# Kernel optimization log

Measured on AMD Instinct MI355X. Metric: run time of the kernel, lower is better.

The kernel has to match this reference:

```python
import jax, jax.numpy as jnp
import numpy as np


def setup_inputs() -> dict:
    key = jax.random.key(0)
    B, N, D = 8, 2048, 512
    put = jax.random.normal(key, (B, N, D), dtype=jnp.float32)
    return {"put": put, "k": 16}


def reference(put, k):
    # put: [B, N, D]; k: python int
    B, N, _ = put.shape
    # squared-norm expansion of pairwise Euclidean distance
    xx = jnp.sum(put * put, axis=2, keepdims=True)            # [B, N, 1]
    gram = jnp.einsum('bnd,bmd->bnm', put, put)               # [B, N, N]
    dist2 = xx + jnp.swapaxes(xx, 1, 2) - 2.0 * gram          # [B, N, N]
    dist = jnp.sqrt(jnp.clip(dist2, 0.0))                     # clamp(min=0).sqrt()

    # k nearest (smallest distance): top_k of negated distances
    _, inc = jax.lax.top_k(-dist, k)                          # [B, N, k] int32

    # binary adjacency: out[b, j, inc[b, j, :]] = 1 (vectorized scatter)
    b_idx = jnp.arange(B)[:, None, None]                      # [B,1,1]
    r_idx = jnp.arange(N)[None, :, None]                      # [1,N,1]
    out = jnp.zeros_like(dist).at[b_idx, r_idx, inc].set(1.0)
    return out
```

## Files before the change

### kernel.cpp

```cpp
#include <hip/hip_runtime.h>
#include <cstdint>

#define NN 2048
#define DD 512
#define NB 8
#define NCAND 24

using ull = unsigned long long;
typedef __attribute__((ext_vector_type(8))) short bf16x8;
typedef __attribute__((ext_vector_type(4))) float f32x4;

#define GLOAD_LDS16(g, l)                                                      \
  __builtin_amdgcn_global_load_lds(                                            \
      (const __attribute__((address_space(1))) unsigned int*)(g),              \
      (__attribute__((address_space(3))) unsigned int*)(l), 16, 0, 0)

__device__ inline unsigned short f2bf(float f) {
  unsigned u = __float_as_uint(f);
  unsigned r = u + 0x7FFFu + ((u >> 16) & 1u);
  return (unsigned short)(r >> 16);
}

__global__ __launch_bounds__(256) void knn_prep(const float* __restrict__ put,
                                                float* __restrict__ norms32,
                                                unsigned short* __restrict__ bhalf) {
  const int row  = blockIdx.x * 4 + (threadIdx.x >> 6);
  const int lane = threadIdx.x & 63;
  const float* p = put + (size_t)row * DD + lane * 8;
  float4 x0 = ((const float4*)p)[0];
  float4 x1 = ((const float4*)p)[1];
  double s = (double)x0.x * (double)x0.x + (double)x0.y * (double)x0.y +
             (double)x0.z * (double)x0.z + (double)x0.w * (double)x0.w +
             (double)x1.x * (double)x1.x + (double)x1.y * (double)x1.y +
             (double)x1.z * (double)x1.z + (double)x1.w * (double)x1.w;
  uint4 v;
  v.x = (unsigned)f2bf(x0.x) | ((unsigned)f2bf(x0.y) << 16);
  v.y = (unsigned)f2bf(x0.z) | ((unsigned)f2bf(x0.w) << 16);
  v.z = (unsigned)f2bf(x1.x) | ((unsigned)f2bf(x1.y) << 16);
  v.w = (unsigned)f2bf(x1.z) | ((unsigned)f2bf(x1.w) << 16);
  *((uint4*)(bhalf + (size_t)row * DD) + lane) = v;
#pragma unroll
  for (int m = 1; m < 64; m <<= 1) s += __shfl_xor(s, m, 64);
  if (lane == 0) norms32[row] = (float)s;
}

__global__ __launch_bounds__(256) void knn_gemm(
    const unsigned short* __restrict__ bhalf,
    const float* __restrict__ norms32,
    unsigned short* __restrict__ Sws) {
  __shared__ unsigned short smem[18432];
  unsigned short* As = smem;
  unsigned short* Bs = smem + 4096;

  int idx = blockIdx.x;
  int jt = 0;
  while (idx >= 16 - jt) { idx -= 16 - jt; ++jt; }
  const int mt = jt + idx;

  const int t    = threadIdx.x;
  const int lane = t & 63;
  const int wv   = t >> 6;
  const int q    = lane >> 4;
  const int l15  = lane & 15;
  const int wrow = wv >> 1, wcol = wv & 1;
  const int m0 = mt * 128;
  const int j0 = jt * 128;
  const int b  = blockIdx.y;

  const unsigned short* pb = bhalf + (size_t)b * NN * DD;

  const int rloc = lane >> 2;
  const int kcg  = (lane & 3) ^ ((lane >> 3) & 3);
  const int i0 = 2 * wv, i1 = 2 * wv + 1;
  const unsigned short* gA0 = pb + (size_t)(j0 + 16 * i0 + rloc) * DD + kcg * 8;
  const unsigned short* gA1 = pb + (size_t)(j0 + 16 * i1 + rloc) * DD + kcg * 8;
  const unsigned short* gB0 = pb + (size_t)(m0 + 16 * i0 + rloc) * DD + kcg * 8;
  const unsigned short* gB1 = pb + (size_t)(m0 + 16 * i1 + rloc) * DD + kcg * 8;
  unsigned short* lA0 = As + i0 * 512;
  unsigned short* lA1 = As + i1 * 512;
  unsigned short* lB0 = Bs + i0 * 512;
  unsigned short* lB1 = Bs + i1 * 512;

  const int xsw = (q ^ ((l15 >> 1) & 3)) * 8;

  f32x4 acc[4][4];
  const f32x4 zz = {0.f, 0.f, 0.f, 0.f};
#pragma unroll
  for (int i = 0; i < 4; ++i)
#pragma unroll
    for (int j = 0; j < 4; ++j) acc[i][j] = zz;

  for (int kt = 0; kt < DD; kt += 32) {
    __syncthreads();
    GLOAD_LDS16(gA0, lA0);
    GLOAD_LDS16(gA1, lA1);
    GLOAD_LDS16(gB0, lB0);
    GLOAD_LDS16(gB1, lB1);
    gA0 += 32; gA1 += 32; gB0 += 32; gB1 += 32;
    __syncthreads();

    bf16x8 af[4], bg[4];
#pragma unroll
    for (int f = 0; f < 4; ++f) {
      af[f] = *(const bf16x8*)(As + (wrow * 64 + f * 16 + l15) * 32 + xsw);
      bg[f] = *(const bf16x8*)(Bs + (wcol * 64 + f * 16 + l15) * 32 + xsw);
    }
#pragma unroll
    for (int fi = 0; fi < 4; ++fi)
#pragma unroll
      for (int fj = 0; fj < 4; ++fj)
        acc[fi][fj] = __builtin_amdgcn_mfma_f32_16x16x32_bf16(
            af[fi], bg[fj], acc[fi][fj], 0, 0, 0);
  }

  float xn[4];
#pragma unroll
  for (int fj = 0; fj < 4; ++fj)
    xn[fj] = norms32[(size_t)b * NN + m0 + wcol * 64 + fj * 16 + l15];

  __syncthreads();
  unsigned short* Sl = smem + wv * 4096;
#pragma unroll
  for (int fi = 0; fi < 4; ++fi)
#pragma unroll
    for (int fj = 0; fj < 4; ++fj)
#pragma unroll
      for (int r = 0; r < 4; ++r) {
        float sv = xn[fj] - 2.0f * acc[fi][fj][r] + 2048.0f;
        Sl[(fi * 16 + q * 4 + r) * 64 + fj * 16 + l15] =
            __builtin_bit_cast(unsigned short, (_Float16)sv);
      }

  const size_t row0 = (size_t)(b * NN + j0 + wrow * 64);
#pragma unroll
  for (int it = 0; it < 8; ++it) {
    int i2 = it * 64 + lane;
    int row = i2 >> 3, c8 = i2 & 7;
    uint4 v = *(const uint4*)(Sl + row * 64 + c8 * 8);
    *(uint4*)(Sws + (row0 + row) * NN + m0 + wcol * 64 + c8 * 8) = v;
  }

  if (jt != mt) {
    float xr[16];
#pragma unroll
    for (int fi = 0; fi < 4; ++fi)
#pragma unroll
      for (int r = 0; r < 4; ++r)
        xr[fi * 4 + r] =
            norms32[(size_t)b * NN + j0 + wrow * 64 + fi * 16 + q * 4 + r];

    __syncthreads();
    unsigned short* Mw = smem + wv * 4608;
#pragma unroll
    for (int fi = 0; fi < 4; ++fi)
#pragma unroll
      for (int fj = 0; fj < 4; ++fj)
#pragma unroll
        for (int r = 0; r < 4; ++r) {
          float sv = xr[fi * 4 + r] - 2.0f * acc[fi][fj][r] + 2048.0f;
          Mw[(fj * 16 + l15) * 72 + fi * 16 + q * 4 + r] =
              __builtin_bit_cast(unsigned short, (_Float16)sv);
        }
    const size_t mrow0 = (size_t)(b * NN + m0 + wcol * 64);
#pragma unroll
    for (int it = 0; it < 8; ++it) {
      int i2 = it * 64 + lane;
      int row = i2 >> 3, c8 = i2 & 7;
      uint4 v = *(const uint4*)(Mw + row * 72 + c8 * 8);
      *(uint4*)(Sws + (mrow0 + row) * NN + j0 + wrow * 64 + c8 * 8) = v;
    }
  }
}

__device__ inline void ins8(unsigned (&h)[8], unsigned k) {
#pragma unroll
  for (int p = 0; p < 8; ++p) {
    unsigned lo = min(h[p], k);
    k = max(h[p], k);
    h[p] = lo;
  }
}

__global__ __launch_bounds__(256) void knn_select(
    const unsigned short* __restrict__ Sws,
    const float* __restrict__ put,
    const float* __restrict__ norms32,
    float* __restrict__ out) {
  __shared__ unsigned candL[4][NCAND];
  __shared__ double part[4][NCAND][9];
  __shared__ ull keyL[4][NCAND];
  __shared__ unsigned winL[4][16];

  const int wv   = threadIdx.x >> 6;
  const int lane = threadIdx.x & 63;
  const int R = blockIdx.x * 4 + wv;
  const int b = R >> 11, j = R & (NN - 1);

  unsigned h[8];
#pragma unroll
  for (int p = 0; p < 8; ++p) h[p] = 0xFFFFFFFFu;
  const unsigned short* Srow = Sws + (size_t)R * NN;
#pragma unroll
  for (int i = 0; i < 4; ++i) {
    uint4 u = *(const uint4*)(Srow + i * 512 + lane * 8);
    unsigned base = (unsigned)(i * 512 + lane * 8);
    ins8(h, (u.x << 16) | base);
    ins8(h, (u.x & 0xFFFF0000u) | (base + 1));
    ins8(h, (u.y << 16) | (base + 2));
    ins8(h, (u.y & 0xFFFF0000u) | (base + 3));
    ins8(h, (u.z << 16) | (base + 4));
    ins8(h, (u.z & 0xFFFF0000u) | (base + 5));
    ins8(h, (u.w << 16) | (base + 6));
    ins8(h, (u.w & 0xFFFF0000u) | (base + 7));
  }

  for (int r = 0; r < NCAND; ++r) {
    unsigned w = h[0];
#pragma unroll
    for (int m = 1; m < 64; m <<= 1)
      w = min(w, (unsigned)__shfl_xor((int)w, m, 64));
    if (h[0] == w) {
      candL[wv][r] = w & 0xFFFFu;
#pragma unroll
      for (int p = 0; p < 7; ++p) h[p] = h[p + 1];
      h[7] = 0xFFFFFFFFu;
    }
  }

  const float* panel = put + (size_t)b * NN * DD;
  const float* xjp = panel + (size_t)j * DD + lane * 8;
  float4 xa = ((const float4*)xjp)[0];
  float4 xb = ((const float4*)xjp)[1];
  double x0 = xa.x, x1 = xa.y, x2 = xa.z, x3 = xa.w;
  double x4 = xb.x, x5 = xb.y, x6 = xb.z, x7 = xb.w;

  for (int c0 = 0; c0 < NCAND; c0 += 4) {
    double p[4];
#pragma unroll
    for (int u = 0; u < 4; ++u) {
      int cand = (int)candL[wv][c0 + u];
      const float4* cr = (const float4*)(panel + (size_t)cand * DD + lane * 8);
      float4 ya = cr[0];
      float4 yb = cr[1];
      p[u] = x0 * (double)ya.x + x1 * (double)ya.y + x2 * (double)ya.z +
             x3 * (double)ya.w + x4 * (double)yb.x + x5 * (double)yb.y +
             x6 * (double)yb.z + x7 * (double)yb.w;
    }
#pragma unroll
    for (int u = 0; u < 4; ++u) {
      p[u] += __shfl_xor(p[u], 1, 64);
      p[u] += __shfl_xor(p[u], 2, 64);
      p[u] += __shfl_xor(p[u], 4, 64);
      if ((lane & 7) == 0) part[wv][c0 + u][lane >> 3] = p[u];
    }
  }

  if (lane < NCAND) {
    double dot = part[wv][lane][0] + part[wv][lane][1] + part[wv][lane][2] +
                 part[wv][lane][3] + part[wv][lane][4] + part[wv][lane][5] +
                 part[wv][lane][6] + part[wv][lane][7];
    int cand = (int)candL[wv][lane];
    float g32 = (float)dot;
    float xxm = norms32[(size_t)b * NN + cand];
    float xxj = norms32[(size_t)b * NN + j];
    float s   = __fadd_rn(xxj, xxm);
    float d2  = __fsub_rn(s, __fmul_rn(2.0f, g32));
    d2 = fmaxf(d2, 0.0f);
    float dist = __fsqrt_rn(d2);
    keyL[wv][lane] = ((ull)__float_as_uint(dist) << 32) | (unsigned)cand;
  }
  if (lane < NCAND) {
    ull mine = keyL[wv][lane];
    int rank = 0;
#pragma unroll
    for (int i = 0; i < NCAND; ++i) rank += (keyL[wv][i] < mine) ? 1 : 0;
    if (rank < 16) winL[wv][rank] = (unsigned)(keyL[wv][lane] & 0xFFFFULL);
  }

  unsigned mask = 0;
#pragma unroll
  for (int i = 0; i < 16; ++i) {
    unsigned c = winL[wv][i];
    unsigned own = (((c >> 2) & 63u) == (unsigned)lane) ? 1u : 0u;
    unsigned bit = (((c >> 8) & 7u) << 2) | (c & 3u);
    mask |= own << bit;
  }
  float* orow = out + (size_t)R * NN;
#pragma unroll
  for (int it = 0; it < 8; ++it) {
    float4 v;
    v.x = (float)((mask >> (it * 4 + 0)) & 1u);
    v.y = (float)((mask >> (it * 4 + 1)) & 1u);
    v.z = (float)((mask >> (it * 4 + 2)) & 1u);
    v.w = (float)((mask >> (it * 4 + 3)) & 1u);
    ((float4*)(orow + it * 256))[lane] = v;
  }
}

extern "C" void kernel_launch(void* const* d_in, const int* in_sizes, int n_in,
                              void* d_out, int out_size, void* d_ws, size_t ws_size,
                              hipStream_t stream) {
  const float* put = (const float*)d_in[0];
  float* out = (float*)d_out;

  float* norms32 = (float*)d_ws;
  unsigned short* bhalf = (unsigned short*)((char*)d_ws + 65536);
  unsigned short* Sws =
      (unsigned short*)((char*)d_ws + 65536 + (size_t)NB * NN * DD * 2);

  knn_prep<<<dim3(NB * NN / 4), 256, 0, stream>>>(put, norms32, bhalf);
  knn_gemm<<<dim3(136, NB), 256, 0, stream>>>(bhalf, norms32, Sws);
  knn_select<<<dim3(NB * NN / 4), 256, 0, stream>>>(Sws, put, norms32, out);
}
```

Before: 253.0 us.

## Replace insertion top-8 with sorting networks and extract two minima per wave pass

Per-lane candidate selection now builds four sorted 8-element runs with a sorting network and merges them with bitonic half-merges, replacing 32 sequential insertions into an 8-slot list. The wave-wide extraction now pulls the two smallest keys per butterfly reduction, halving the number of reduction passes for the 24 candidates, and writes candidates from lane 0 only. Candidate indices are read with readfirstlane so the gather addresses become scalar. This lowers ALU and shuffle work in the select kernel at the cost of more live registers.

```diff
diff --git a/kernel.cpp b/kernel.cpp
--- a/kernel.cpp
+++ b/kernel.cpp
@@ -172,13 +172,42 @@
   }
 }
 
-__device__ inline void ins8(unsigned (&h)[8], unsigned k) {
-#pragma unroll
-  for (int p = 0; p < 8; ++p) {
-    unsigned lo = min(h[p], k);
-    k = max(h[p], k);
-    h[p] = lo;
-  }
+#define CEX(a, i, j)                                                           \
+  {                                                                            \
+    unsigned lo_ = min(a[i], a[j]), hi_ = max(a[i], a[j]);                     \
+    a[i] = lo_;                                                                \
+    a[j] = hi_;                                                                \
+  }
+
+__device__ inline void mk8(unsigned (&a)[8], uint4 u, unsigned base) {
+  a[0] = (u.x << 16) | base;
+  a[1] = (u.x & 0xFFFF0000u) | (base + 1);
+  a[2] = (u.y << 16) | (base + 2);
+  a[3] = (u.y & 0xFFFF0000u) | (base + 3);
+  a[4] = (u.z << 16) | (base + 4);
+  a[5] = (u.z & 0xFFFF0000u) | (base + 5);
+  a[6] = (u.w << 16) | (base + 6);
+  a[7] = (u.w & 0xFFFF0000u) | (base + 7);
+}
+
+__device__ inline void sort8(unsigned (&a)[8]) {
+  CEX(a, 0, 1) CEX(a, 2, 3) CEX(a, 4, 5) CEX(a, 6, 7)
+  CEX(a, 0, 2) CEX(a, 1, 3) CEX(a, 4, 6) CEX(a, 5, 7)
+  CEX(a, 1, 2) CEX(a, 5, 6)
+  CEX(a, 0, 4) CEX(a, 1, 5) CEX(a, 2, 6) CEX(a, 3, 7)
+  CEX(a, 2, 4) CEX(a, 3, 5)
+  CEX(a, 1, 2) CEX(a, 3, 4) CEX(a, 5, 6)
+}
+
+__device__ inline void merge8(unsigned (&a)[8], const unsigned (&b)[8]) {
+  unsigned t[8];
+#pragma unroll
+  for (int i = 0; i < 8; ++i) t[i] = min(a[i], b[7 - i]);
+  CEX(t, 0, 4) CEX(t, 1, 5) CEX(t, 2, 6) CEX(t, 3, 7)
+  CEX(t, 0, 2) CEX(t, 1, 3) CEX(t, 4, 6) CEX(t, 5, 7)
+  CEX(t, 0, 1) CEX(t, 2, 3) CEX(t, 4, 5) CEX(t, 6, 7)
+#pragma unroll
+  for (int i = 0; i < 8; ++i) a[i] = t[i];
 }
 
 __global__ __launch_bounds__(256) void knn_select(
@@ -196,34 +225,47 @@
   const int R = blockIdx.x * 4 + wv;
   const int b = R >> 11, j = R & (NN - 1);
 
-  unsigned h[8];
-#pragma unroll
-  for (int p = 0; p < 8; ++p) h[p] = 0xFFFFFFFFu;
   const unsigned short* Srow = Sws + (size_t)R * NN;
-#pragma unroll
-  for (int i = 0; i < 4; ++i) {
-    uint4 u = *(const uint4*)(Srow + i * 512 + lane * 8);
-    unsigned base = (unsigned)(i * 512 + lane * 8);
-    ins8(h, (u.x << 16) | base);
-    ins8(h, (u.x & 0xFFFF0000u) | (base + 1));
-    ins8(h, (u.y << 16) | (base + 2));
-    ins8(h, (u.y & 0xFFFF0000u) | (base + 3));
-    ins8(h, (u.z << 16) | (base + 4));
-    ins8(h, (u.z & 0xFFFF0000u) | (base + 5));
-    ins8(h, (u.w << 16) | (base + 6));
-    ins8(h, (u.w & 0xFFFF0000u) | (base + 7));
-  }
-
-  for (int r = 0; r < NCAND; ++r) {
-    unsigned w = h[0];
-#pragma unroll
-    for (int m = 1; m < 64; m <<= 1)
-      w = min(w, (unsigned)__shfl_xor((int)w, m, 64));
-    if (h[0] == w) {
-      candL[wv][r] = w & 0xFFFFu;
+  uint4 u0 = *(const uint4*)(Srow + 0 * 512 + lane * 8);
+  uint4 u1 = *(const uint4*)(Srow + 1 * 512 + lane * 8);
+  uint4 u2 = *(const uint4*)(Srow + 2 * 512 + lane * 8);
+  uint4 u3 = *(const uint4*)(Srow + 3 * 512 + lane * 8);
+  unsigned h[8], c1[8], c2[8], c3[8];
+  mk8(h, u0, (unsigned)(0 * 512 + lane * 8));
+  mk8(c1, u1, (unsigned)(1 * 512 + lane * 8));
+  mk8(c2, u2, (unsigned)(2 * 512 + lane * 8));
+  mk8(c3, u3, (unsigned)(3 * 512 + lane * 8));
+  sort8(h); sort8(c1); sort8(c2); sort8(c3);
+  merge8(h, c1);
+  merge8(c2, c3);
+  merge8(h, c2);
+
+#pragma unroll
+  for (int pass = 0; pass < NCAND / 2; ++pass) {
+    unsigned a1 = h[0], a2 = h[1];
+#pragma unroll
+    for (int m = 1; m < 64; m <<= 1) {
+      unsigned b1 = (unsigned)__shfl_xor((int)a1, m, 64);
+      unsigned b2 = (unsigned)__shfl_xor((int)a2, m, 64);
+      unsigned lo  = min(a1, b1);
+      unsigned mid = max(a1, b1);
+      unsigned hi  = min(a2, b2);
+      a1 = lo;
+      a2 = min(mid, hi);
+    }
+    if ((h[0] == a1) | (h[0] == a2)) {
 #pragma unroll
       for (int p = 0; p < 7; ++p) h[p] = h[p + 1];
       h[7] = 0xFFFFFFFFu;
+    }
+    if (h[0] == a2) {
+#pragma unroll
+      for (int p = 0; p < 7; ++p) h[p] = h[p + 1];
+      h[7] = 0xFFFFFFFFu;
+    }
+    if (lane == 0) {
+      candL[wv][2 * pass]     = a1 & 0xFFFFu;
+      candL[wv][2 * pass + 1] = a2 & 0xFFFFu;
     }
   }
 
@@ -237,21 +279,21 @@
   for (int c0 = 0; c0 < NCAND; c0 += 4) {
     double p[4];
 #pragma unroll
-    for (int u = 0; u < 4; ++u) {
-      int cand = (int)candL[wv][c0 + u];
+    for (int uu = 0; uu < 4; ++uu) {
+      int cand = __builtin_amdgcn_readfirstlane((int)candL[wv][c0 + uu]);
       const float4* cr = (const float4*)(panel + (size_t)cand * DD + lane * 8);
       float4 ya = cr[0];
       float4 yb = cr[1];
-      p[u] = x0 * (double)ya.x + x1 * (double)ya.y + x2 * (double)ya.z +
-             x3 * (double)ya.w + x4 * (double)yb.x + x5 * (double)yb.y +
-             x6 * (double)yb.z + x7 * (double)yb.w;
-    }
-#pragma unroll
-    for (int u = 0; u < 4; ++u) {
-      p[u] += __shfl_xor(p[u], 1, 64);
-      p[u] += __shfl_xor(p[u], 2, 64);
-      p[u] += __shfl_xor(p[u], 4, 64);
-      if ((lane & 7) == 0) part[wv][c0 + u][lane >> 3] = p[u];
+      p[uu] = x0 * (double)ya.x + x1 * (double)ya.y + x2 * (double)ya.z +
+              x3 * (double)ya.w + x4 * (double)yb.x + x5 * (double)yb.y +
+              x6 * (double)yb.z + x7 * (double)yb.w;
+    }
+#pragma unroll
+    for (int uu = 0; uu < 4; ++uu) {
+      p[uu] += __shfl_xor(p[uu], 1, 64);
+      p[uu] += __shfl_xor(p[uu], 2, 64);
+      p[uu] += __shfl_xor(p[uu], 4, 64);
+      if ((lane & 7) == 0) part[wv][c0 + uu][lane >> 3] = p[uu];
     }
   }
 
```

Measured after the change: 248.5 us. Within noise of the previous version (-1.8%).
